# Kernel tuning notes

Measured on AMD Instinct MI355X. Metric: run time of the kernel, lower is better.

## Reference

```python
import jax, jax.numpy as jnp
import numpy as np

B, L, D, K, NFFT = 4, 8192, 768, 24, 16384


def setup_inputs() -> dict:
    key = jax.random.key(0)
    k1, k2, k3, k4 = jax.random.split(key, 4)
    x = jax.random.normal(k1, (B, L, D), dtype=jnp.float32)
    phi = jax.random.normal(k2, (L, K), dtype=jnp.float32) * 0.1
    M_inputs = jax.random.normal(k3, (D, D), dtype=jnp.float32) * 0.02
    M_filters = jax.random.normal(k4, (K, D), dtype=jnp.float32) * 0.02
    return {"x": x, "phi": phi, "M_inputs": M_inputs, "M_filters": M_filters, "n": NFFT}


def _convolve_approx(u, v, n):
    # u: (B, L, D) projected inputs; v: (L, D) projected filters (per-channel kernels)
    bsz, seq_len, d = u.shape
    sgn = jnp.where(jnp.arange(seq_len) % 2 == 0, 1.0, -1.0).astype(u.dtype)[None, :, None]  # (1,L,1)
    V = jnp.fft.rfft(v.astype(jnp.float32), n=n, axis=0)[None, :, :, None]  # (1,F,D,1)
    U = jnp.stack([u, u * sgn], axis=-1).astype(jnp.float32)  # (B,L,D,2): [plus, sign-flipped]
    Uf = jnp.fft.rfft(U, n=n, axis=1)  # (B,F,D,2)
    conv = jnp.fft.irfft(V * Uf, n=n, axis=1)[:, :seq_len]  # (B,L,D,2)
    U_plus = conv[..., 0]
    U_minus = conv[..., 1] * sgn
    return U_plus, U_minus


def reference(x, phi, M_inputs, M_filters, n):
    x_proj = x @ M_inputs          # (B,L,D)
    phi_proj = phi @ M_filters     # (L,D)
    spectral_plus, spectral_minus = _convolve_approx(x_proj, phi_proj, n)
    return spectral_plus + spectral_minus
```

## Files before the change

### kernel.cpp

```cpp
#include <hip/hip_runtime.h>
#include <stdint.h>

#define B_SZ 4
#define L_SEQ 8192
#define D_CH 768
#define K_F 24
#define NFFT2 8192
#define LDS_BYTES 69632
#define GEMM_LDS 98304

typedef __attribute__((ext_vector_type(4))) float f32x4;
typedef __attribute__((ext_vector_type(8))) __bf16 bf16x8;

__device__ __forceinline__ uint32_t f2bf1(float f) {
  uint32_t u = __float_as_uint(f);
  return (u + 0x7fffu + ((u >> 16) & 1u)) >> 16;
}
__device__ __forceinline__ uint32_t packbf2(float lo, float hi) {
  return f2bf1(lo) | (f2bf1(hi) << 16);
}
__device__ __forceinline__ float2 unpackbf2(uint32_t v) {
  return float2{__uint_as_float(v << 16), __uint_as_float(v & 0xffff0000u)};
}
__device__ __forceinline__ float2 cmulf(float2 a, float2 b) {
  return float2{a.x * b.x - a.y * b.y, a.x * b.y + a.y * b.x};
}
__device__ __forceinline__ uint32_t pkbf(float lo, float hi) {
  uint32_t r;
  asm("v_cvt_pk_bf16_f32 %0, %1, %2" : "=v"(r) : "v"(lo), "v"(hi));
  return r;
}

__global__ __launch_bounds__(256) void k_mit(const float* __restrict__ Mi,
                                             uint16_t* __restrict__ MiT) {
  int i = blockIdx.x * 256 + threadIdx.x;
  int n = i / 768, e = i - n * 768;
  MiT[i] = (uint16_t)f2bf1(Mi[e * 768 + n]);
}

template <int S>
__device__ __forceinline__ void dft8(float2* x) {
  const float C = 0.70710678118654752f;
  float2 t0{x[0].x + x[4].x, x[0].y + x[4].y}, t1{x[0].x - x[4].x, x[0].y - x[4].y};
  float2 t2{x[2].x + x[6].x, x[2].y + x[6].y}, t3{x[2].x - x[6].x, x[2].y - x[6].y};
  float2 t4{x[1].x + x[5].x, x[1].y + x[5].y}, t5{x[1].x - x[5].x, x[1].y - x[5].y};
  float2 t6{x[3].x + x[7].x, x[3].y + x[7].y}, t7{x[3].x - x[7].x, x[3].y - x[7].y};
  float2 t3r = (S < 0) ? float2{t3.y, -t3.x} : float2{-t3.y, t3.x};
  float2 t7r = (S < 0) ? float2{t7.y, -t7.x} : float2{-t7.y, t7.x};
  float2 e0{t0.x + t2.x, t0.y + t2.y}, e2{t0.x - t2.x, t0.y - t2.y};
  float2 e1{t1.x + t3r.x, t1.y + t3r.y}, e3{t1.x - t3r.x, t1.y - t3r.y};
  float2 o0{t4.x + t6.x, t4.y + t6.y}, o2{t4.x - t6.x, t4.y - t6.y};
  float2 o1{t5.x + t7r.x, t5.y + t7r.y}, o3{t5.x - t7r.x, t5.y - t7r.y};
  float2 o1r = (S < 0) ? float2{C * (o1.x + o1.y), C * (o1.y - o1.x)}
                       : float2{C * (o1.x - o1.y), C * (o1.y + o1.x)};
  float2 o2r = (S < 0) ? float2{o2.y, -o2.x} : float2{-o2.y, o2.x};
  float2 o3r = (S < 0) ? float2{C * (o3.y - o3.x), -C * (o3.x + o3.y)}
                       : float2{-C * (o3.x + o3.y), C * (o3.x - o3.y)};
  x[0] = float2{e0.x + o0.x, e0.y + o0.y};
  x[4] = float2{e0.x - o0.x, e0.y - o0.y};
  x[1] = float2{e1.x + o1r.x, e1.y + o1r.y};
  x[5] = float2{e1.x - o1r.x, e1.y - o1r.y};
  x[2] = float2{e2.x + o2r.x, e2.y + o2r.y};
  x[6] = float2{e2.x - o2r.x, e2.y - o2r.y};
  x[3] = float2{e3.x + o3r.x, e3.y + o3r.y};
  x[7] = float2{e3.x - o3r.x, e3.y - o3r.y};
}

template <int LH, int S, int NT>
__device__ __forceinline__ void pass_r8(float2* a, int tid) {
  constexpr int h = 1 << LH;
  constexpr int st = h + (h >> 4);
  const float ang = (S < 0 ? -6.2831853071795864769f : 6.2831853071795864769f) / (float)(h * 8);
  __syncthreads();
#pragma unroll
  for (int jj = 0; jj < 1024 / NT; ++jj) {
    int j = jj * NT + tid;
    int pos = j & (h - 1);
    int base = ((j >> LH) << (LH + 3)) + pos;
    float2* p = a + (base + (base >> 4));
    float2 x[8];
#pragma unroll
    for (int q = 0; q < 8; ++q) x[q] = p[q * st];
    float sn, cs;
    __sincosf(ang * (float)pos, &sn, &cs);
    float2 w{cs, sn};
    if constexpr (S < 0) {
      dft8<-1>(x);
      float2 wq = w;
      x[1] = cmulf(x[1], wq);
#pragma unroll
      for (int q = 2; q < 8; ++q) {
        wq = cmulf(wq, w);
        x[q] = cmulf(x[q], wq);
      }
    } else {
      float2 wq = w;
      x[1] = cmulf(x[1], wq);
#pragma unroll
      for (int q = 2; q < 8; ++q) {
        wq = cmulf(wq, w);
        x[q] = cmulf(x[q], wq);
      }
      dft8<1>(x);
    }
#pragma unroll
    for (int q = 0; q < 8; ++q) p[q * st] = x[q];
  }
}

__device__ __forceinline__ void p1_fused(float2* a, const uint32_t* __restrict__ row32, int tid) {
#pragma unroll
  for (int jj = 0; jj < 2; ++jj) {
    int j = jj * 512 + tid;
    float2 x[8];
#pragma unroll
    for (int q = 0; q < 4; ++q) x[q] = unpackbf2(row32[j + q * 1024]);
    x[4] = x[5] = x[6] = x[7] = float2{0.f, 0.f};
    dft8<-1>(x);
    float sn, cs;
    __sincosf(-6.2831853071795864769f / 8192.0f * (float)j, &sn, &cs);
    float2 w{cs, sn}, wq = w;
    x[1] = cmulf(x[1], wq);
#pragma unroll
    for (int q = 2; q < 8; ++q) {
      wq = cmulf(wq, w);
      x[q] = cmulf(x[q], wq);
    }
    float2* p = a + (j + (j >> 4));
#pragma unroll
    for (int q = 0; q < 8; ++q) p[q * 1088] = x[q];
  }
}

__device__ __forceinline__ void mid_fused(float2* a, const uint32_t* __restrict__ wrow, int tid) {
  __syncthreads();
#pragma unroll
  for (int jj = 0; jj < 8; ++jj) {
    int j = jj * 512 + tid;
    float2* p = a + (2 * j + ((2 * j) >> 4));
    float2 u = p[0], v = p[1];
    float2 s{u.x + v.x, u.y + v.y}, dd{u.x - v.x, u.y - v.y};
    uint2 wv = *(const uint2*)(wrow + 2 * j);
    s = cmulf(s, unpackbf2(wv.x));
    dd = cmulf(dd, unpackbf2(wv.y));
    p[0] = float2{s.x + dd.x, s.y + dd.y};
    p[1] = float2{s.x - dd.x, s.y - dd.y};
  }
}

__device__ __forceinline__ void last_fused(float2* a, uint32_t* __restrict__ out32, int tid) {
  __syncthreads();
#pragma unroll
  for (int jj = 0; jj < 2; ++jj) {
    int j = jj * 512 + tid;
    float2* p = a + (j + (j >> 4));
    float2 x[8];
#pragma unroll
    for (int q = 0; q < 8; ++q) x[q] = p[q * 1088];
    float sn, cs;
    __sincosf(6.2831853071795864769f / 8192.0f * (float)j, &sn, &cs);
    float2 w{cs, sn}, wq = w;
    x[1] = cmulf(x[1], wq);
#pragma unroll
    for (int q = 2; q < 8; ++q) {
      wq = cmulf(wq, w);
      x[q] = cmulf(x[q], wq);
    }
    dft8<1>(x);
#pragma unroll
    for (int q = 0; q < 4; ++q) out32[j + q * 1024] = packbf2(x[q].x, x[q].y);
  }
}

__global__ __launch_bounds__(256) void k_phi(const float* __restrict__ phi,
                                             float2* __restrict__ Phi2) {
  extern __shared__ float2 buf[];
  int k = blockIdx.x, tid = threadIdx.x;
  const float scale = 2.0f / 8192.0f;
  for (int r = tid; r < 4096; r += 256) {
    buf[r + (r >> 4)] = float2{phi[(2 * r) * K_F + k] * scale, 0.0f};
    int r2i = r + 4096;
    buf[r2i + (r2i >> 4)] = float2{0.0f, 0.0f};
  }
  pass_r8<10, -1, 256>(buf, tid);
  pass_r8<7, -1, 256>(buf, tid);
  pass_r8<4, -1, 256>(buf, tid);
  pass_r8<1, -1, 256>(buf, tid);
  __syncthreads();
  for (int j = tid; j < 4096; j += 256) {
    float2* p = buf + (2 * j + ((2 * j) >> 4));
    float2 u = p[0], v = p[1];
    p[0] = float2{u.x + v.x, u.y + v.y};
    p[1] = float2{u.x - v.x, u.y - v.y};
  }
  __syncthreads();
  for (int f = tid; f < NFFT2; f += 256) Phi2[k * NFFT2 + f] = buf[f + (f >> 4)];
}

__global__ __launch_bounds__(256) void k_w2(const float2* __restrict__ Phi2,
                                            const float* __restrict__ Mf,
                                            uint32_t* __restrict__ W2) {
  __shared__ float2 p[K_F][256];
  __shared__ float mf[K_F][32];
  int tid = threadIdx.x;
  int fc = blockIdx.x & 31, dc = blockIdx.x >> 5;
  int f0 = fc * 256, d0 = dc * 32;
  for (int i = tid; i < K_F * 256; i += 256) {
    int k = i >> 8, fl = i & 255;
    p[k][fl] = Phi2[k * NFFT2 + f0 + fl];
  }
  for (int i = tid; i < K_F * 32; i += 256) {
    int k = i >> 5, dl = i & 31;
    mf[k][dl] = Mf[k * D_CH + d0 + dl];
  }
  __syncthreads();
  for (int dl = 0; dl < 32; ++dl) {
    float re = 0.f, im = 0.f;
#pragma unroll
    for (int k = 0; k < K_F; ++k) {
      float m = mf[k][dl];
      re += m * p[k][tid].x;
      im += m * p[k][tid].y;
    }
    W2[(size_t)(d0 + dl) * NFFT2 + f0 + tid] = packbf2(re, im);
  }
}

__device__ __forceinline__ void gload_lds16(const void* g, void* l) {
  __builtin_amdgcn_global_load_lds(
      (const __attribute__((address_space(1))) void*)g,
      (__attribute__((address_space(3))) void*)l, 16, 0, 0);
}

__global__ __launch_bounds__(512, 2) void k_gemm(const float* __restrict__ X,
                                                 const uint16_t* __restrict__ MiT,
                                                 uint16_t* __restrict__ Cp) {
  extern __shared__ char lds[];
  char* const As0 = lds;
  char* const Bs0 = lds + 32768;
  int tid = threadIdx.x;
  int lane = tid & 63, wid = tid >> 6;
  int p = blockIdx.x;
  int v = (p & 7) * 96 + (p >> 3);
  int bm = v / 3, bn = v % 3;
  int m0 = bm * 128, n0 = bn * 256;
  int wr = wid >> 2, wc = wid & 3;
  int lm = lane & 15, lg = lane >> 4;
  f32x4 acc[4][4] = {};
  float4 fa[4];

#define STAGE_B(bufc, k0)                                              \
  _Pragma("unroll") for (int it = 0; it < 4; ++it) {                   \
    int s = it * 512 + tid;                                            \
    int row = s >> 3;                                                  \
    int cb = ((s & 7) << 4) ^ ((row & 7) << 4);                        \
    gload_lds16(MiT + (size_t)(n0 + row) * 768 + (k0) + (cb >> 1),     \
                Bs0 + (bufc)*32768 + (it * 512 + wid * 64) * 16);      \
  }
#define LOAD_A(k0)                                                     \
  _Pragma("unroll") for (int jt = 0; jt < 2; ++jt) {                   \
    int s = jt * 512 + tid;                                            \
    int row = s >> 3, c16 = s & 7;                                     \
    const float* src = X + (size_t)(m0 + row) * 768 + (k0) + c16 * 8;  \
    fa[2 * jt] = *(const float4*)src;                                  \
    fa[2 * jt + 1] = *(const float4*)(src + 4);                        \
  }
#define WRITE_A(bufc)                                                  \
  _Pragma("unroll") for (int jt = 0; jt < 2; ++jt) {                   \
    int s = jt * 512 + tid;                                            \
    int row = s >> 3, c16 = s & 7;                                     \
    uint4 o;                                                           \
    o.x = pkbf(fa[2 * jt].x, fa[2 * jt].y);                            \
    o.y = pkbf(fa[2 * jt].z, fa[2 * jt].w);                            \
    o.z = pkbf(fa[2 * jt + 1].x, fa[2 * jt + 1].y);                    \
    o.w = pkbf(fa[2 * jt + 1].z, fa[2 * jt + 1].w);                    \
    *(uint4*)(As0 + (bufc)*16384 + row * 128 + ((c16 << 4) ^ ((row & 7) << 4))) = o; \
  }
#define RD_A(dst, bufc, kbyte)                                                         \
  _Pragma("unroll") for (int i = 0; i < 4; ++i) {                                      \
    int row = wr * 64 + i * 16 + lm;                                                   \
    dst[i] = *(const bf16x8*)(As0 + (bufc)*16384 + row * 128 + ((kbyte) ^ ((row & 7) << 4))); \
  }
#define RD_B(dst, bufc, kbyte)                                                         \
  _Pragma("unroll") for (int i = 0; i < 4; ++i) {                                      \
    int row = wc * 64 + i * 16 + lm;                                                   \
    dst[i] = *(const bf16x8*)(Bs0 + (bufc)*32768 + row * 128 + ((kbyte) ^ ((row & 7) << 4))); \
  }
#define MFMA16(av, bv)                                                        \
  _Pragma("unroll") for (int mi = 0; mi < 4; ++mi)                            \
  _Pragma("unroll") for (int ni = 0; ni < 4; ++ni)                            \
      acc[mi][ni] = __builtin_amdgcn_mfma_f32_16x16x32_bf16(av[mi], bv[ni], acc[mi][ni], 0, 0, 0);

  STAGE_B(0, 0);
  LOAD_A(0);
  WRITE_A(0);
  asm volatile("s_waitcnt vmcnt(0) lgkmcnt(0)" ::: "memory");
  __builtin_amdgcn_s_barrier();

  int cur = 0;
  for (int kt = 0; kt < 12; ++kt) {
    int nxt = cur ^ 1, k0n = (kt + 1) * 64;
    int kb0 = lg * 16, kb1 = 64 + lg * 16;
    if (kt < 11) {
      STAGE_B(nxt, k0n);
      LOAD_A(k0n);
    }
    {
      bf16x8 a0[4], b0[4];
      RD_A(a0, cur, kb0);
      RD_B(b0, cur, kb0);
      asm volatile("s_waitcnt lgkmcnt(0)" ::: "memory");
      __builtin_amdgcn_sched_barrier(0);
      __builtin_amdgcn_s_setprio(1);
      MFMA16(a0, b0);
      __builtin_amdgcn_s_setprio(0);
    }
    __builtin_amdgcn_s_barrier();
    {
      bf16x8 a1[4], b1[4];
      RD_A(a1, cur, kb1);
      RD_B(b1, cur, kb1);
      asm volatile("s_waitcnt lgkmcnt(0)" ::: "memory");
      __builtin_amdgcn_sched_barrier(0);
      __builtin_amdgcn_s_setprio(1);
      MFMA16(a1, b1);
      __builtin_amdgcn_s_setprio(0);
    }
    if (kt < 11) WRITE_A(nxt);
    asm volatile("s_waitcnt vmcnt(0) lgkmcnt(0)" ::: "memory");
    __builtin_amdgcn_s_barrier();
    cur = nxt;
  }
#undef STAGE_B
#undef LOAD_A
#undef WRITE_A
#undef RD_A
#undef RD_B
#undef MFMA16

#pragma unroll
  for (int mi = 0; mi < 4; ++mi) {
#pragma unroll
    for (int ni = 0; ni < 4; ++ni) {
      int mg = m0 + wr * 64 + mi * 16 + lg * 4;
      int dd = n0 + wc * 64 + ni * 16 + lm;
      int bb = mg >> 13, t = mg & 8191;
      f32x4 vv = acc[mi][ni];
      uint2 o;
      o.x = packbf2(vv[0], vv[1]);
      o.y = packbf2(vv[2], vv[3]);
      *(uint2*)(Cp + ((size_t)bb * 768 + dd) * 8192 + t) = o;
    }
  }
}

__global__ __launch_bounds__(512, 4) void k_conv(const uint16_t* __restrict__ xprojT,
                                                 const uint32_t* __restrict__ W2,
                                                 uint16_t* __restrict__ convo) {
  extern __shared__ float2 buf[];
  int tid = threadIdx.x;
  int bd = blockIdx.x;
  int d = bd % 768;
  const uint32_t* row32 = (const uint32_t*)(xprojT + (size_t)bd * 8192);
  p1_fused(buf, row32, tid);
  pass_r8<7, -1, 512>(buf, tid);
  pass_r8<4, -1, 512>(buf, tid);
  pass_r8<1, -1, 512>(buf, tid);
  mid_fused(buf, W2 + (size_t)d * NFFT2, tid);
  pass_r8<1, 1, 512>(buf, tid);
  pass_r8<4, 1, 512>(buf, tid);
  pass_r8<7, 1, 512>(buf, tid);
  last_fused(buf, (uint32_t*)(convo + (size_t)bd * 8192), tid);
}

__global__ __launch_bounds__(256) void k_tr(const uint16_t* __restrict__ convo,
                                            float* __restrict__ out) {
  __shared__ uint16_t tile[64][72];
  int tid = threadIdx.x;
  int bx = blockIdx.x;
  int b = bx / 1536;
  int r = bx - b * 1536;
  int d0 = (r >> 7) << 6;
  int t0 = (r & 127) << 6;
  {
    int rr = tid >> 3;
    int c8 = (tid & 7) << 3;
#pragma unroll
    for (int p = 0; p < 2; ++p) {
      int row = p * 32 + rr;
      uint4 v = *(const uint4*)(convo + ((size_t)(b * 768 + d0 + row)) * 8192 + t0 + c8);
      *(uint4*)&tile[row][c8] = v;
    }
  }
  __syncthreads();
  {
    int c4 = (tid & 15) << 2;
    int tg = tid >> 4;
#pragma unroll
    for (int p = 0; p < 4; ++p) {
      int tt = p * 16 + tg;
      float4 o;
      o.x = __uint_as_float((uint32_t)tile[c4 + 0][tt] << 16);
      o.y = __uint_as_float((uint32_t)tile[c4 + 1][tt] << 16);
      o.z = __uint_as_float((uint32_t)tile[c4 + 2][tt] << 16);
      o.w = __uint_as_float((uint32_t)tile[c4 + 3][tt] << 16);
      *(float4*)(out + ((size_t)b * 8192 + t0 + tt) * 768 + d0 + c4) = o;
    }
  }
}

extern "C" void kernel_launch(void* const* d_in, const int* in_sizes, int n_in,
                              void* d_out, int out_size, void* d_ws, size_t ws_size,
                              hipStream_t stream) {
  const float* x   = (const float*)d_in[0];
  const float* phi = (const float*)d_in[1];
  const float* Mi  = (const float*)d_in[2];
  const float* Mf  = (const float*)d_in[3];
  float* out = (float*)d_out;

  uint16_t* xprojT = (uint16_t*)d_out + 25165824;

  char* ws = (char*)d_ws;
  uint16_t* convo = (uint16_t*)ws;
  uint32_t* W2    = (uint32_t*)(ws + 50331648);
  float2*   Phi2  = (float2*)(ws + 75497472);
  uint16_t* MiT   = (uint16_t*)(ws + 77070336);

  k_mit<<<2304, 256, 0, stream>>>(Mi, MiT);
  k_phi<<<24, 256, LDS_BYTES, stream>>>(phi, Phi2);
  k_w2<<<768, 256, 0, stream>>>(Phi2, Mf, W2);
  k_gemm<<<768, 512, GEMM_LDS, stream>>>(x, MiT, xprojT);
  k_conv<<<3072, 512, LDS_BYTES, stream>>>(xprojT, W2, convo);
  k_tr<<<6144, 256, 0, stream>>>(convo, out);
}
```

Measured before the change: 230.1 us.

## Use precomputed twiddle tables in FFTs and triple-buffer GEMM B/A prefetch

Adds a kernel that fills a double-precision-derived twiddle table in the output buffer, and the FFT passes load all seven twiddles per butterfly instead of doing sincos plus chained complex multiplies. This removes transcendental and dependent multiply work and improves twiddle accuracy, at the cost of extra global loads per butterfly. Separately, the GEMM main loop is reworked to triple-buffer B in LDS and keep three A register sets in flight, with partial vmcnt waits and one barrier fewer per iteration, to hide global latency. This uses more LDS (131072 bytes) and more registers, which may lower occupancy.

```diff
diff --git a/kernel.cpp b/kernel.cpp
--- a/kernel.cpp
+++ b/kernel.cpp
@@ -7,10 +7,16 @@
 #define K_F 24
 #define NFFT2 8192
 #define LDS_BYTES 69632
-#define GEMM_LDS 98304
+#define GEMM_LDS 131072
 
 typedef __attribute__((ext_vector_type(4))) float f32x4;
 typedef __attribute__((ext_vector_type(8))) __bf16 bf16x8;
+
+#define TW1024 0
+#define TW128 8192
+#define TW16 9216
+#define TW2 9344
+#define TW_TOTAL 9360
 
 __device__ __forceinline__ uint32_t f2bf1(float f) {
   uint32_t u = __float_as_uint(f);
@@ -24,11 +30,27 @@
 }
 __device__ __forceinline__ float2 cmulf(float2 a, float2 b) {
   return float2{a.x * b.x - a.y * b.y, a.x * b.y + a.y * b.x};
+}
+__device__ __forceinline__ float2 cmulc(float2 a, float2 b) {
+  return float2{a.x * b.x + a.y * b.y, a.y * b.x - a.x * b.y};
 }
 __device__ __forceinline__ uint32_t pkbf(float lo, float hi) {
   uint32_t r;
   asm("v_cvt_pk_bf16_f32 %0, %1, %2" : "=v"(r) : "v"(lo), "v"(hi));
   return r;
+}
+
+__global__ __launch_bounds__(256) void k_tw(float2* __restrict__ TW) {
+  int i = blockIdx.x * 256 + threadIdx.x;
+  if (i >= TW_TOTAL) return;
+  int e = i >> 3, q = i & 7;
+  int h, pos;
+  if (e < 1024) { h = 1024; pos = e; }
+  else if (e < 1152) { h = 128; pos = e - 1024; }
+  else if (e < 1168) { h = 16; pos = e - 1152; }
+  else { h = 2; pos = e - 1168; }
+  double ang = -6.28318530717958647692 * (double)(pos * q) / (double)(8 * h);
+  TW[i] = float2{(float)cos(ang), (float)sin(ang)};
 }
 
 __global__ __launch_bounds__(256) void k_mit(const float* __restrict__ Mi,
@@ -66,11 +88,16 @@
   x[7] = float2{e3.x - o3r.x, e3.y - o3r.y};
 }
 
+#define TWLOAD(tw, pos)                                            \
+  const float4* tp_ = (const float4*)((tw) + ((size_t)(pos) << 3)); \
+  float4 t01 = tp_[0], t23 = tp_[1], t45 = tp_[2], t67 = tp_[3];   \
+  float2 w1{t01.z, t01.w}, w2{t23.x, t23.y}, w3{t23.z, t23.w},     \
+      w4{t45.x, t45.y}, w5{t45.z, t45.w}, w6{t67.x, t67.y}, w7{t67.z, t67.w};
+
 template <int LH, int S, int NT>
-__device__ __forceinline__ void pass_r8(float2* a, int tid) {
+__device__ __forceinline__ void pass_r8t(float2* a, const float2* __restrict__ tw, int tid) {
   constexpr int h = 1 << LH;
   constexpr int st = h + (h >> 4);
-  const float ang = (S < 0 ? -6.2831853071795864769f : 6.2831853071795864769f) / (float)(h * 8);
   __syncthreads();
 #pragma unroll
   for (int jj = 0; jj < 1024 / NT; ++jj) {
@@ -78,29 +105,19 @@
     int pos = j & (h - 1);
     int base = ((j >> LH) << (LH + 3)) + pos;
     float2* p = a + (base + (base >> 4));
+    TWLOAD(tw, pos);
     float2 x[8];
 #pragma unroll
     for (int q = 0; q < 8; ++q) x[q] = p[q * st];
-    float sn, cs;
-    __sincosf(ang * (float)pos, &sn, &cs);
-    float2 w{cs, sn};
     if constexpr (S < 0) {
       dft8<-1>(x);
-      float2 wq = w;
-      x[1] = cmulf(x[1], wq);
-#pragma unroll
-      for (int q = 2; q < 8; ++q) {
-        wq = cmulf(wq, w);
-        x[q] = cmulf(x[q], wq);
-      }
+      x[1] = cmulf(x[1], w1); x[2] = cmulf(x[2], w2); x[3] = cmulf(x[3], w3);
+      x[4] = cmulf(x[4], w4); x[5] = cmulf(x[5], w5); x[6] = cmulf(x[6], w6);
+      x[7] = cmulf(x[7], w7);
     } else {
-      float2 wq = w;
-      x[1] = cmulf(x[1], wq);
-#pragma unroll
-      for (int q = 2; q < 8; ++q) {
-        wq = cmulf(wq, w);
-        x[q] = cmulf(x[q], wq);
-      }
+      x[1] = cmulc(x[1], w1); x[2] = cmulc(x[2], w2); x[3] = cmulc(x[3], w3);
+      x[4] = cmulc(x[4], w4); x[5] = cmulc(x[5], w5); x[6] = cmulc(x[6], w6);
+      x[7] = cmulc(x[7], w7);
       dft8<1>(x);
     }
 #pragma unroll
@@ -108,24 +125,20 @@
   }
 }
 
-__device__ __forceinline__ void p1_fused(float2* a, const uint32_t* __restrict__ row32, int tid) {
+__device__ __forceinline__ void p1_fused(float2* a, const uint32_t* __restrict__ row32,
+                                         const float2* __restrict__ tw, int tid) {
 #pragma unroll
   for (int jj = 0; jj < 2; ++jj) {
     int j = jj * 512 + tid;
+    TWLOAD(tw, j);
     float2 x[8];
 #pragma unroll
     for (int q = 0; q < 4; ++q) x[q] = unpackbf2(row32[j + q * 1024]);
     x[4] = x[5] = x[6] = x[7] = float2{0.f, 0.f};
     dft8<-1>(x);
-    float sn, cs;
-    __sincosf(-6.2831853071795864769f / 8192.0f * (float)j, &sn, &cs);
-    float2 w{cs, sn}, wq = w;
-    x[1] = cmulf(x[1], wq);
-#pragma unroll
-    for (int q = 2; q < 8; ++q) {
-      wq = cmulf(wq, w);
-      x[q] = cmulf(x[q], wq);
-    }
+    x[1] = cmulf(x[1], w1); x[2] = cmulf(x[2], w2); x[3] = cmulf(x[3], w3);
+    x[4] = cmulf(x[4], w4); x[5] = cmulf(x[5], w5); x[6] = cmulf(x[6], w6);
+    x[7] = cmulf(x[7], w7);
     float2* p = a + (j + (j >> 4));
 #pragma unroll
     for (int q = 0; q < 8; ++q) p[q * 1088] = x[q];
@@ -148,24 +161,20 @@
   }
 }
 
-__device__ __forceinline__ void last_fused(float2* a, uint32_t* __restrict__ out32, int tid) {
+__device__ __forceinline__ void last_fused(float2* a, uint32_t* __restrict__ out32,
+                                           const float2* __restrict__ tw, int tid) {
   __syncthreads();
 #pragma unroll
   for (int jj = 0; jj < 2; ++jj) {
     int j = jj * 512 + tid;
+    TWLOAD(tw, j);
     float2* p = a + (j + (j >> 4));
     float2 x[8];
 #pragma unroll
     for (int q = 0; q < 8; ++q) x[q] = p[q * 1088];
-    float sn, cs;
-    __sincosf(6.2831853071795864769f / 8192.0f * (float)j, &sn, &cs);
-    float2 w{cs, sn}, wq = w;
-    x[1] = cmulf(x[1], wq);
-#pragma unroll
-    for (int q = 2; q < 8; ++q) {
-      wq = cmulf(wq, w);
-      x[q] = cmulf(x[q], wq);
-    }
+    x[1] = cmulc(x[1], w1); x[2] = cmulc(x[2], w2); x[3] = cmulc(x[3], w3);
+    x[4] = cmulc(x[4], w4); x[5] = cmulc(x[5], w5); x[6] = cmulc(x[6], w6);
+    x[7] = cmulc(x[7], w7);
     dft8<1>(x);
 #pragma unroll
     for (int q = 0; q < 4; ++q) out32[j + q * 1024] = packbf2(x[q].x, x[q].y);
@@ -173,6 +182,7 @@
 }
 
 __global__ __launch_bounds__(256) void k_phi(const float* __restrict__ phi,
+                                             const float2* __restrict__ TW,
                                              float2* __restrict__ Phi2) {
   extern __shared__ float2 buf[];
   int k = blockIdx.x, tid = threadIdx.x;
@@ -182,10 +192,10 @@
     int r2i = r + 4096;
     buf[r2i + (r2i >> 4)] = float2{0.0f, 0.0f};
   }
-  pass_r8<10, -1, 256>(buf, tid);
-  pass_r8<7, -1, 256>(buf, tid);
-  pass_r8<4, -1, 256>(buf, tid);
-  pass_r8<1, -1, 256>(buf, tid);
+  pass_r8t<10, -1, 256>(buf, TW + TW1024, tid);
+  pass_r8t<7, -1, 256>(buf, TW + TW128, tid);
+  pass_r8t<4, -1, 256>(buf, TW + TW16, tid);
+  pass_r8t<1, -1, 256>(buf, TW + TW2, tid);
   __syncthreads();
   for (int j = tid; j < 4096; j += 256) {
     float2* p = buf + (2 * j + ((2 * j) >> 4));
@@ -240,14 +250,14 @@
   char* const Bs0 = lds + 32768;
   int tid = threadIdx.x;
   int lane = tid & 63, wid = tid >> 6;
-  int p = blockIdx.x;
-  int v = (p & 7) * 96 + (p >> 3);
+  int pb = blockIdx.x;
+  int v = (pb & 7) * 96 + (pb >> 3);
   int bm = v / 3, bn = v % 3;
   int m0 = bm * 128, n0 = bn * 256;
   int wr = wid >> 2, wc = wid & 3;
   int lm = lane & 15, lg = lane >> 4;
   f32x4 acc[4][4] = {};
-  float4 fa[4];
+  float4 fa[3][4];
 
 #define STAGE_B(bufc, k0)                                              \
   _Pragma("unroll") for (int it = 0; it < 4; ++it) {                   \
@@ -255,36 +265,36 @@
     int row = s >> 3;                                                  \
     int cb = ((s & 7) << 4) ^ ((row & 7) << 4);                        \
     gload_lds16(MiT + (size_t)(n0 + row) * 768 + (k0) + (cb >> 1),     \
-                Bs0 + (bufc)*32768 + (it * 512 + wid * 64) * 16);      \
-  }
-#define LOAD_A(k0)                                                     \
+                Bs0 + (bufc) * 32768 + (it * 512 + wid * 64) * 16);    \
+  }
+#define LOAD_A(aset, k0)                                               \
   _Pragma("unroll") for (int jt = 0; jt < 2; ++jt) {                   \
     int s = jt * 512 + tid;                                            \
     int row = s >> 3, c16 = s & 7;                                     \
     const float* src = X + (size_t)(m0 + row) * 768 + (k0) + c16 * 8;  \
-    fa[2 * jt] = *(const float4*)src;                                  \
-    fa[2 * jt + 1] = *(const float4*)(src + 4);                        \
-  }
-#define WRITE_A(bufc)                                                  \
+    fa[aset][2 * jt] = *(const float4*)src;                            \
+    fa[aset][2 * jt + 1] = *(const float4*)(src + 4);                  \
+  }
+#define WRITE_A(abuf, aset)                                            \
   _Pragma("unroll") for (int jt = 0; jt < 2; ++jt) {                   \
     int s = jt * 512 + tid;                                            \
     int row = s >> 3, c16 = s & 7;                                     \
     uint4 o;                                                           \
-    o.x = pkbf(fa[2 * jt].x, fa[2 * jt].y);                            \
-    o.y = pkbf(fa[2 * jt].z, fa[2 * jt].w);                            \
-    o.z = pkbf(fa[2 * jt + 1].x, fa[2 * jt + 1].y);                    \
-    o.w = pkbf(fa[2 * jt + 1].z, fa[2 * jt + 1].w);                    \
-    *(uint4*)(As0 + (bufc)*16384 + row * 128 + ((c16 << 4) ^ ((row & 7) << 4))) = o; \
-  }
-#define RD_A(dst, bufc, kbyte)                                                         \
-  _Pragma("unroll") for (int i = 0; i < 4; ++i) {                                      \
-    int row = wr * 64 + i * 16 + lm;                                                   \
-    dst[i] = *(const bf16x8*)(As0 + (bufc)*16384 + row * 128 + ((kbyte) ^ ((row & 7) << 4))); \
-  }
-#define RD_B(dst, bufc, kbyte)                                                         \
-  _Pragma("unroll") for (int i = 0; i < 4; ++i) {                                      \
-    int row = wc * 64 + i * 16 + lm;                                                   \
-    dst[i] = *(const bf16x8*)(Bs0 + (bufc)*32768 + row * 128 + ((kbyte) ^ ((row & 7) << 4))); \
+    o.x = pkbf(fa[aset][2 * jt].x, fa[aset][2 * jt].y);                \
+    o.y = pkbf(fa[aset][2 * jt].z, fa[aset][2 * jt].w);                \
+    o.z = pkbf(fa[aset][2 * jt + 1].x, fa[aset][2 * jt + 1].y);        \
+    o.w = pkbf(fa[aset][2 * jt + 1].z, fa[aset][2 * jt + 1].w);        \
+    *(uint4*)(As0 + (abuf) * 16384 + row * 128 + ((c16 << 4) ^ ((row & 7) << 4))) = o; \
+  }
+#define RD_A(dst, abuf, kbyte)                                                              \
+  _Pragma("unroll") for (int i = 0; i < 4; ++i) {                                           \
+    int row = wr * 64 + i * 16 + lm;                                                        \
+    dst[i] = *(const bf16x8*)(As0 + (abuf) * 16384 + row * 128 + ((kbyte) ^ ((row & 7) << 4))); \
+  }
+#define RD_B(dst, bufc, kbyte)                                                              \
+  _Pragma("unroll") for (int i = 0; i < 4; ++i) {                                           \
+    int row = wc * 64 + i * 16 + lm;                                                        \
+    dst[i] = *(const bf16x8*)(Bs0 + (bufc) * 32768 + row * 128 + ((kbyte) ^ ((row & 7) << 4))); \
   }
 #define MFMA16(av, bv)                                                        \
   _Pragma("unroll") for (int mi = 0; mi < 4; ++mi)                            \
@@ -292,44 +302,47 @@
       acc[mi][ni] = __builtin_amdgcn_mfma_f32_16x16x32_bf16(av[mi], bv[ni], acc[mi][ni], 0, 0, 0);
 
   STAGE_B(0, 0);
-  LOAD_A(0);
-  WRITE_A(0);
-  asm volatile("s_waitcnt vmcnt(0) lgkmcnt(0)" ::: "memory");
+  LOAD_A(0, 0);
+  STAGE_B(1, 64);
+  LOAD_A(1, 64);
+  LOAD_A(2, 128);
+  WRITE_A(0, 0);
+  asm volatile("s_waitcnt lgkmcnt(0)" ::: "memory");
   __builtin_amdgcn_s_barrier();
 
-  int cur = 0;
+  int kb0 = lg * 16, kb1 = 64 + lg * 16;
+#pragma unroll
   for (int kt = 0; kt < 12; ++kt) {
-    int nxt = cur ^ 1, k0n = (kt + 1) * 64;
-    int kb0 = lg * 16, kb1 = 64 + lg * 16;
-    if (kt < 11) {
-      STAGE_B(nxt, k0n);
-      LOAD_A(k0n);
-    }
+    if (kt <= 9) STAGE_B((kt + 2) % 3, (kt + 2) * 64);
+    if (kt <= 8) LOAD_A((kt + 3) % 3, (kt + 3) * 64);
     {
       bf16x8 a0[4], b0[4];
-      RD_A(a0, cur, kb0);
-      RD_B(b0, cur, kb0);
+      RD_A(a0, kt & 1, kb0);
+      RD_B(b0, kt % 3, kb0);
       asm volatile("s_waitcnt lgkmcnt(0)" ::: "memory");
       __builtin_amdgcn_sched_barrier(0);
       __builtin_amdgcn_s_setprio(1);
       MFMA16(a0, b0);
       __builtin_amdgcn_s_setprio(0);
     }
-    __builtin_amdgcn_s_barrier();
     {
       bf16x8 a1[4], b1[4];
-      RD_A(a1, cur, kb1);
-      RD_B(b1, cur, kb1);
+      RD_A(a1, kt & 1, kb1);
+      RD_B(b1, kt % 3, kb1);
       asm volatile("s_waitcnt lgkmcnt(0)" ::: "memory");
       __builtin_amdgcn_sched_barrier(0);
       __builtin_amdgcn_s_setprio(1);
       MFMA16(a1, b1);
       __builtin_amdgcn_s_setprio(0);
     }
-    if (kt < 11) WRITE_A(nxt);
-    asm volatile("s_waitcnt vmcnt(0) lgkmcnt(0)" ::: "memory");
-    __builtin_amdgcn_s_barrier();
-    cur = nxt;
+    if (kt <= 10) {
+      WRITE_A((kt + 1) & 1, (kt + 1) % 3);
+      if (kt <= 8)      asm volatile("s_waitcnt vmcnt(12)" ::: "memory");
+      else if (kt == 9) asm volatile("s_waitcnt vmcnt(8)" ::: "memory");
+      else              asm volatile("s_waitcnt vmcnt(0)" ::: "memory");
+      asm volatile("s_waitcnt lgkmcnt(0)" ::: "memory");
+      __builtin_amdgcn_s_barrier();
+    }
   }
 #undef STAGE_B
 #undef LOAD_A
@@ -356,21 +369,22 @@
 
 __global__ __launch_bounds__(512, 4) void k_conv(const uint16_t* __restrict__ xprojT,
                                                  const uint32_t* __restrict__ W2,
+                                                 const float2* __restrict__ TW,
                                                  uint16_t* __restrict__ convo) {
   extern __shared__ float2 buf[];
   int tid = threadIdx.x;
   int bd = blockIdx.x;
   int d = bd % 768;
   const uint32_t* row32 = (const uint32_t*)(xprojT + (size_t)bd * 8192);
-  p1_fused(buf, row32, tid);
-  pass_r8<7, -1, 512>(buf, tid);
-  pass_r8<4, -1, 512>(buf, tid);
-  pass_r8<1, -1, 512>(buf, tid);
+  p1_fused(buf, row32, TW + TW1024, tid);
+  pass_r8t<7, -1, 512>(buf, TW + TW128, tid);
+  pass_r8t<4, -1, 512>(buf, TW + TW16, tid);
+  pass_r8t<1, -1, 512>(buf, TW + TW2, tid);
   mid_fused(buf, W2 + (size_t)d * NFFT2, tid);
-  pass_r8<1, 1, 512>(buf, tid);
-  pass_r8<4, 1, 512>(buf, tid);
-  pass_r8<7, 1, 512>(buf, tid);
-  last_fused(buf, (uint32_t*)(convo + (size_t)bd * 8192), tid);
+  pass_r8t<1, 1, 512>(buf, TW + TW2, tid);
+  pass_r8t<4, 1, 512>(buf, TW + TW16, tid);
+  pass_r8t<7, 1, 512>(buf, TW + TW128, tid);
+  last_fused(buf, (uint32_t*)(convo + (size_t)bd * 8192), TW + TW1024, tid);
 }
 
 __global__ __launch_bounds__(256) void k_tr(const uint16_t* __restrict__ convo,
@@ -418,6 +432,7 @@
   const float* Mf  = (const float*)d_in[3];
   float* out = (float*)d_out;
 
+  float2* TW = (float2*)d_out;
   uint16_t* xprojT = (uint16_t*)d_out + 25165824;
 
   char* ws = (char*)d_ws;
@@ -426,10 +441,11 @@
   float2*   Phi2  = (float2*)(ws + 75497472);
   uint16_t* MiT   = (uint16_t*)(ws + 77070336);
 
+  k_tw<<<(TW_TOTAL + 255) / 256, 256, 0, stream>>>(TW);
   k_mit<<<2304, 256, 0, stream>>>(Mi, MiT);
-  k_phi<<<24, 256, LDS_BYTES, stream>>>(phi, Phi2);
+  k_phi<<<24, 256, LDS_BYTES, stream>>>(phi, TW, Phi2);
   k_w2<<<768, 256, 0, stream>>>(Phi2, Mf, W2);
   k_gemm<<<768, 512, GEMM_LDS, stream>>>(x, MiT, xprojT);
-  k_conv<<<3072, 512, LDS_BYTES, stream>>>(xprojT, W2, convo);
+  k_conv<<<3072, 512, LDS_BYTES, stream>>>(xprojT, W2, TW, convo);
   k_tr<<<6144, 256, 0, stream>>>(convo, out);
 }
```

New measurement: 337.3 us. 1.47x slower.
